# Performance work log

Hardware: AMD Instinct MI355X
Metric: run time of the kernel (lower is better)

Reference implementation:

```python
import jax, jax.numpy as jnp
import numpy as np

B, L, D, H = 2, 2048, 1024, 16
DK = D // H


def setup_inputs() -> dict:
    key = jax.random.key(0)
    ks = jax.random.split(key, 11)
    s = 1.0 / np.sqrt(D)
    inp = {
        "context_sequence": jax.random.normal(ks[0], (B, L, D), jnp.float32),
        "value_sequence": jax.random.normal(ks[1], (B, L, D), jnp.float32),
        "mask": jnp.tril(jnp.ones((L, L), jnp.int32)),  # causal mask [L, L]
        "Wq": jax.random.normal(ks[2], (D, D), jnp.float32) * s,
        "bq": jax.random.normal(ks[3], (D,), jnp.float32) * s,
        "Wk": jax.random.normal(ks[4], (D, D), jnp.float32) * s,
        "bk": jax.random.normal(ks[5], (D,), jnp.float32) * s,
        "Wv": jax.random.normal(ks[6], (D, D), jnp.float32) * s,
        "bv": jax.random.normal(ks[7], (D,), jnp.float32) * s,
        "Wo": jax.random.normal(ks[8], (D, D), jnp.float32) * s,
        "bo": jax.random.normal(ks[9], (D,), jnp.float32) * s,
    }
    return inp


def reference(context_sequence, value_sequence, mask, Wq, bq, Wk, bk, Wv, bv, Wo, bo):
    orig_dtype = context_sequence.dtype
    # QKV projections; Q,K from context, V from value stream
    Q = (context_sequence @ Wq + bq).reshape(B, L, H, DK)
    K = (context_sequence @ Wk + bk).reshape(B, L, H, DK)
    V = (value_sequence @ Wv + bv).reshape(B, L, H, DK)
    # fp32 QK^T with 1/sqrt(d_k) scaling -> [B, H, L, L]
    scores = jnp.einsum("bqhd,bkhd->bhqk", Q.astype(jnp.float32), K.astype(jnp.float32)) / jnp.sqrt(
        jnp.asarray(DK, jnp.float32)
    )
    # dtype-dependent neg fill (fp32 -> -inf); causal rows always have >=1 valid entry
    neg_fill = jnp.asarray(-jnp.inf, jnp.float32)
    scores = jnp.where(mask[None, None, :, :] == 0, neg_fill, scores)
    scores = scores.astype(orig_dtype)
    attn = jax.nn.softmax(scores, axis=-1)
    # dropout is identity in eval mode
    out = jnp.einsum("bhqk,bkhd->bqhd", attn, V).reshape(B, L, D)
    return out @ Wo + bo
```

## Files before the change

### kernel.cpp

```cpp
#include <hip/hip_runtime.h>
#include <hip/hip_bf16.h>
#include <stdint.h>

#define B_   2
#define L_   2048
#define D_   1024
#define H_   16
#define DK_  64

typedef __attribute__((ext_vector_type(4))) float f32x4;
typedef __attribute__((ext_vector_type(8))) short short8;
typedef unsigned short ushort_t;

__device__ __forceinline__ ushort_t f2bf(float f) {
    union { float f; uint32_t u; } v; v.f = f;
    uint32_t r = v.u + 0x7FFFu + ((v.u >> 16) & 1u);
    return (ushort_t)(r >> 16);
}
__device__ __forceinline__ float bf2f(ushort_t u) {
    union { uint32_t u; float f; } v; v.u = (uint32_t)u << 16; return v.f;
}
__device__ __forceinline__ uint32_t pack_bf16_rne(float a, float b) {
    return (uint32_t)f2bf(a) | ((uint32_t)f2bf(b) << 16);
}

__device__ __forceinline__ void async_copy16(void* lds, const void* g) {
    __builtin_amdgcn_global_load_lds(
        (const __attribute__((address_space(1))) uint32_t*)g,
        (__attribute__((address_space(3))) uint32_t*)lds, 16, 0, 0);
}

__global__ void prep_kernel(const float* __restrict__ ctx, const float* __restrict__ val,
                            const float* __restrict__ w0, const float* __restrict__ w1,
                            const float* __restrict__ w2, const float* __restrict__ w3,
                            ushort_t* __restrict__ xc, ushort_t* __restrict__ xv,
                            ushort_t* __restrict__ wt) {
    __shared__ float tile[32][33];
    const int bid = blockIdx.x;
    if (bid < 8192) {
        const float* s = (bid >= 4096) ? val : ctx;
        ushort_t*    d = (bid >= 4096) ? xv : xc;
        int i = ((bid & 4095) * 256 + threadIdx.x) * 4;
        float4 v = *(const float4*)(s + i);
        ushort4 o;
        o.x = f2bf(v.x); o.y = f2bf(v.y); o.z = f2bf(v.z); o.w = f2bf(v.w);
        *(ushort4*)(d + i) = o;
    } else {
        const int t = bid - 8192;
        const int z = t >> 10;
        const int rem = t & 1023;
        const int by = rem >> 5, bx = rem & 31;
        const float* w = (z == 0) ? w0 : (z == 1) ? w1 : (z == 2) ? w2 : w3;
        ushort_t* o = wt + (size_t)z * D_ * D_;
        const int tx = threadIdx.x & 31, ty = threadIdx.x >> 5;
        const int k0 = by * 32, d0 = bx * 32;
#pragma unroll
        for (int i = 0; i < 4; i++)
            tile[ty + i * 8][tx] = w[(size_t)(k0 + ty + i * 8) * D_ + d0 + tx];
        __syncthreads();
#pragma unroll
        for (int i = 0; i < 4; i++)
            o[(size_t)(d0 + ty + i * 8) * D_ + k0 + tx] = f2bf(tile[tx][ty + i * 8]);
    }
}

template <bool SWAP>
__device__ __forceinline__ void gemm_main(const ushort_t* __restrict__ A,
                                          const ushort_t* __restrict__ WT,
                                          char* smem, int m0, int n0, int tid,
                                          f32x4 (&acc)[4][4]) {
    const int wid = tid >> 6, lane = tid & 63;
    const int wm = (wid >> 1) * 64, wn = (wid & 1) * 64;
#pragma unroll
    for (int i = 0; i < 4; i++)
#pragma unroll
        for (int j = 0; j < 4; j++) { f32x4 z = {0.f, 0.f, 0.f, 0.f}; acc[i][j] = z; }

    auto stage = [&](int buf, int k0) {
        char* bA = smem + buf * 32768;
        char* bB = bA + 16384;
#pragma unroll
        for (int i = 0; i < 4; i++) {
            int flat = i * 256 + tid; int row = flat >> 3; int win = (flat & 7) * 16;
            const char* srcA = (const char*)A + ((size_t)(m0 + row) * D_ + k0) * 2 + (win ^ ((row & 7) << 4));
            async_copy16(bA + (i * 256 + wid * 64) * 16, srcA);
            const char* srcB = (const char*)WT + ((size_t)(n0 + row) * D_ + k0) * 2 + (win ^ ((row & 7) << 4));
            async_copy16(bB + (i * 256 + wid * 64) * 16, srcB);
        }
    };

    stage(0, 0);
    int cur = 0;
    for (int k0 = 0; k0 < D_; k0 += 64) {
        __syncthreads();
        if (k0 + 64 < D_) stage(cur ^ 1, k0 + 64);
        const char* bA = smem + cur * 32768;
        const char* bB = bA + 16384;
#pragma unroll
        for (int ks = 0; ks < 2; ks++) {
            short8 af[4], bf[4];
            int kb = ks * 64 + ((lane >> 4) << 4);
#pragma unroll
            for (int t = 0; t < 4; t++) {
                int ml = wm + t * 16 + (lane & 15);
                af[t] = *(const short8*)(bA + ml * 128 + (kb ^ ((ml & 7) << 4)));
                int nl = wn + t * 16 + (lane & 15);
                bf[t] = *(const short8*)(bB + nl * 128 + (kb ^ ((nl & 7) << 4)));
            }
#pragma unroll
            for (int mt = 0; mt < 4; mt++)
#pragma unroll
                for (int nt = 0; nt < 4; nt++)
                    acc[mt][nt] = SWAP
                        ? __builtin_amdgcn_mfma_f32_16x16x32_bf16(bf[nt], af[mt], acc[mt][nt], 0, 0, 0)
                        : __builtin_amdgcn_mfma_f32_16x16x32_bf16(af[mt], bf[nt], acc[mt][nt], 0, 0, 0);
        }
        cur ^= 1;
    }
}

__device__ __forceinline__ void gemm_main8(const ushort_t* __restrict__ A,
                                           const ushort_t* __restrict__ WT,
                                           char* smem, int m0, int n0, int tid,
                                           f32x4 (&acc)[4][2]) {
    const int wid = tid >> 6, lane = tid & 63;
    const int wm = (wid >> 2) * 64, wn = (wid & 3) * 32;
#pragma unroll
    for (int i = 0; i < 4; i++)
#pragma unroll
        for (int j = 0; j < 2; j++) { f32x4 z = {0.f, 0.f, 0.f, 0.f}; acc[i][j] = z; }

    auto stage = [&](int buf, int k0) {
        char* bA = smem + buf * 32768;
        char* bB = bA + 16384;
#pragma unroll
        for (int i = 0; i < 2; i++) {
            int flat = i * 512 + tid; int row = flat >> 3; int win = (flat & 7) * 16;
            const char* srcA = (const char*)A + ((size_t)(m0 + row) * D_ + k0) * 2 + (win ^ ((row & 7) << 4));
            async_copy16(bA + (i * 512 + wid * 64) * 16, srcA);
            const char* srcB = (const char*)WT + ((size_t)(n0 + row) * D_ + k0) * 2 + (win ^ ((row & 7) << 4));
            async_copy16(bB + (i * 512 + wid * 64) * 16, srcB);
        }
    };

    stage(0, 0);
    int cur = 0;
    for (int k0 = 0; k0 < D_; k0 += 64) {
        __syncthreads();
        if (k0 + 64 < D_) stage(cur ^ 1, k0 + 64);
        const char* bA = smem + cur * 32768;
        const char* bB = bA + 16384;
#pragma unroll
        for (int ks = 0; ks < 2; ks++) {
            short8 af[4], bf[2];
            int kb = ks * 64 + ((lane >> 4) << 4);
#pragma unroll
            for (int t = 0; t < 4; t++) {
                int ml = wm + t * 16 + (lane & 15);
                af[t] = *(const short8*)(bA + ml * 128 + (kb ^ ((ml & 7) << 4)));
            }
#pragma unroll
            for (int t = 0; t < 2; t++) {
                int nl = wn + t * 16 + (lane & 15);
                bf[t] = *(const short8*)(bB + nl * 128 + (kb ^ ((nl & 7) << 4)));
            }
#pragma unroll
            for (int mt = 0; mt < 4; mt++)
#pragma unroll
                for (int nt = 0; nt < 2; nt++)
                    acc[mt][nt] = __builtin_amdgcn_mfma_f32_16x16x32_bf16(bf[nt], af[mt], acc[mt][nt], 0, 0, 0);
        }
        cur ^= 1;
    }
}

#define QSCALE 0.18033688f

__global__ __launch_bounds__(256, 2) void gemm_qkv(
    const ushort_t* __restrict__ Xc, const ushort_t* __restrict__ Xv,
    const ushort_t* __restrict__ WT0,
    const float* __restrict__ bq, const float* __restrict__ bk, const float* __restrict__ bv,
    ushort_t* __restrict__ qw, ushort_t* __restrict__ kw, ushort_t* __restrict__ vtw) {
    __shared__ __align__(16) char smem[65536];
    const int z = blockIdx.z;
    const ushort_t* A  = (z == 2) ? Xv : Xc;
    const ushort_t* WT = WT0 + (size_t)z * D_ * D_;
    const float* bias  = (z == 0) ? bq : (z == 1) ? bk : bv;
    const int tid = threadIdx.x, wid = tid >> 6, lane = tid & 63;
    const int lo = lane & 15, hi = lane >> 4;
    const int m0 = blockIdx.y * 128, n0 = blockIdx.x * 128;
    const int wm = (wid >> 1) * 64, wn = (wid & 1) * 64;
    f32x4 acc[4][4];
    if (z != 2) {
        gemm_main<true>(A, WT, smem, m0, n0, tid, acc);
#pragma unroll
        for (int mt = 0; mt < 4; mt++)
#pragma unroll
            for (int nt = 0; nt < 4; nt++) {
                int m  = m0 + wm + mt * 16 + lo;
                int nb = n0 + wn + nt * 16 + 4 * hi;
                float4 b4 = *(const float4*)(bias + nb);
                float v0 = acc[mt][nt][0] + b4.x;
                float v1 = acc[mt][nt][1] + b4.y;
                float v2 = acc[mt][nt][2] + b4.z;
                float v3 = acc[mt][nt][3] + b4.w;
                if (z == 0) { v0 *= QSCALE; v1 *= QSCALE; v2 *= QSCALE; v3 *= QSCALE; }
                int b = m >> 11, tok = m & 2047, h = nb >> 6, dk = nb & 63;
                uint2 w;
                w.x = pack_bf16_rne(v0, v1);
                w.y = pack_bf16_rne(v2, v3);
                ushort_t* outp = (z == 0) ? qw : kw;
                *(uint2*)(outp + ((size_t)(b * H_ + h) * L_ + tok) * DK_ + dk) = w;
            }
    } else {
        gemm_main<false>(A, WT, smem, m0, n0, tid, acc);
#pragma unroll
        for (int mt = 0; mt < 4; mt++)
#pragma unroll
            for (int nt = 0; nt < 4; nt++) {
                int n  = n0 + wn + nt * 16 + lo;
                int mb = m0 + wm + mt * 16 + 4 * hi;
                float bv_ = bias[n];
                int b = mb >> 11, tok = mb & 2047, h = n >> 6, dk = n & 63;
                uint2 w;
                w.x = pack_bf16_rne(acc[mt][nt][0] + bv_, acc[mt][nt][1] + bv_);
                w.y = pack_bf16_rne(acc[mt][nt][2] + bv_, acc[mt][nt][3] + bv_);
                *(uint2*)(vtw + ((size_t)(b * H_ + h) * DK_ + dk) * L_ + tok) = w;
            }
    }
}

__global__ __launch_bounds__(512, 2) void gemm_out(
    const ushort_t* __restrict__ O, const ushort_t* __restrict__ WT,
    const float* __restrict__ bo, float* __restrict__ out) {
    __shared__ __align__(16) char smem[65536];
    const int tid = threadIdx.x, wid = tid >> 6, lane = tid & 63;
    const int lo = lane & 15, hi = lane >> 4;
    const int m0 = blockIdx.y * 128, n0 = blockIdx.x * 128;
    const int wm = (wid >> 2) * 64, wn = (wid & 3) * 32;
    f32x4 acc[4][2];
    gemm_main8(O, WT, smem, m0, n0, tid, acc);
#pragma unroll
    for (int mt = 0; mt < 4; mt++)
#pragma unroll
        for (int nt = 0; nt < 2; nt++) {
            int m  = m0 + wm + mt * 16 + lo;
            int nb = n0 + wn + nt * 16 + 4 * hi;
            float4 b4 = *(const float4*)(bo + nb);
            float4 o;
            o.x = acc[mt][nt][0] + b4.x;
            o.y = acc[mt][nt][1] + b4.y;
            o.z = acc[mt][nt][2] + b4.z;
            o.w = acc[mt][nt][3] + b4.w;
            *(float4*)(out + (size_t)m * D_ + nb) = o;
        }
}

__global__ __launch_bounds__(512, 2) void attn_kernel(
    const ushort_t* __restrict__ qws, const ushort_t* __restrict__ kws,
    const ushort_t* __restrict__ vtws, ushort_t* __restrict__ ows) {
    __shared__ __align__(16) char smem[67584];
    const int tid = threadIdx.x, wid = tid >> 6, lane = tid & 63;
    const int lo = lane & 15, hi = lane >> 4;
    const int bid = blockIdx.x;
    const int xcd = bid & 7, slot = bid >> 3;
    const int bh = xcd * 4 + (slot >> 4);
    const int pi = slot & 15;
    char* P0 = smem + wid * 8192;
    float* lall = (float*)(smem + 65536);
    float* lw = lall + wid * 64;
    const int swz = (lo & 7) << 4;

    short8 ones;
#pragma unroll
    for (int i = 0; i < 8; i++) ones[i] = (short)0x3F80;
    const f32x4 minit = {-32.f, -32.f, -32.f, -32.f};

#pragma unroll 1
    for (int half = 0; half < 2; half++) {
        const int qtb = half ? (31 - pi) : pi;
        const int Q0 = qtb * 64;
        const int ntiles = qtb + 1;

        short8 qf[4][2];
#pragma unroll
        for (int qt = 0; qt < 4; qt++)
#pragma unroll
            for (int ks = 0; ks < 2; ks++)
                qf[qt][ks] = *(const short8*)(qws + (size_t)(bh * L_ + Q0 + qt * 16 + lo) * DK_ + ks * 32 + hi * 8);

        f32x4 oa[4][4];
        f32x4 lf4[4];
#pragma unroll
        for (int qt = 0; qt < 4; qt++) {
            f32x4 z = {0.f, 0.f, 0.f, 0.f};
            lf4[qt] = z;
#pragma unroll
            for (int ot = 0; ot < 4; ot++) oa[qt][ot] = z;
        }

#pragma unroll 1
        for (int t = wid; t < ntiles; t += 8) {
            const int k0 = t * 64;
            const bool diag = (t == qtb);
            short8 vf[4][2];
#pragma unroll
            for (int ot = 0; ot < 4; ot++)
#pragma unroll
                for (int ks = 0; ks < 2; ks++)
                    vf[ot][ks] = *(const short8*)(vtws + (size_t)(bh * DK_ + ot * 16 + lo) * L_ + k0 + ks * 32 + hi * 8);
#pragma unroll
            for (int kt = 0; kt < 4; kt++) {
                const ushort_t* krow = kws + (size_t)(bh * L_ + k0 + kt * 16 + lo) * DK_ + hi * 8;
                short8 kf0 = *(const short8*)(krow);
                short8 kf1 = *(const short8*)(krow + 32);
                const int kb = kt * 16 + 4 * hi;
#pragma unroll
                for (int qt = 0; qt < 4; qt++) {
                    f32x4 s = __builtin_amdgcn_mfma_f32_16x16x32_bf16(kf0, qf[qt][0], minit, 0, 0, 0);
                    s = __builtin_amdgcn_mfma_f32_16x16x32_bf16(kf1, qf[qt][1], s, 0, 0, 0);
                    float p0 = __builtin_amdgcn_exp2f(s[0]);
                    float p1 = __builtin_amdgcn_exp2f(s[1]);
                    float p2 = __builtin_amdgcn_exp2f(s[2]);
                    float p3 = __builtin_amdgcn_exp2f(s[3]);
                    if (diag) {
                        const int qg = qt * 16 + lo;
                        p0 = (kb > qg)     ? 0.f : p0;
                        p1 = (kb + 1 > qg) ? 0.f : p1;
                        p2 = (kb + 2 > qg) ? 0.f : p2;
                        p3 = (kb + 3 > qg) ? 0.f : p3;
                    }
                    uint2 w;
                    w.x = __builtin_amdgcn_perm(__float_as_uint(p1), __float_as_uint(p0), 0x07060302u);
                    w.y = __builtin_amdgcn_perm(__float_as_uint(p3), __float_as_uint(p2), 0x07060302u);
                    *(uint2*)(P0 + qt * 2048 + lo * 128 + ((kt * 32 + hi * 8) ^ swz)) = w;
                }
            }
            __builtin_amdgcn_s_setprio(1);
#pragma unroll
            for (int qt = 0; qt < 4; qt++)
#pragma unroll
                for (int ks = 0; ks < 2; ks++) {
                    short8 pf = *(const short8*)(P0 + qt * 2048 + lo * 128 + ((ks * 64 + hi * 16) ^ swz));
                    lf4[qt] = __builtin_amdgcn_mfma_f32_16x16x32_bf16(pf, ones, lf4[qt], 0, 0, 0);
#pragma unroll
                    for (int ot = 0; ot < 4; ot++)
                        oa[qt][ot] = __builtin_amdgcn_mfma_f32_16x16x32_bf16(pf, vf[ot][ks], oa[qt][ot], 0, 0, 0);
                }
            __builtin_amdgcn_s_setprio(0);
        }

#pragma unroll
        for (int qt = 0; qt < 4; qt++)
#pragma unroll
            for (int ot = 0; ot < 4; ot++)
#pragma unroll
                for (int r = 0; r < 4; r++) {
                    int row = qt * 16 + 4 * hi + r;
                    *(ushort_t*)(P0 + row * 128 + (((ot * 16 + lo) * 2) ^ ((row & 7) << 4))) = f2bf(oa[qt][ot][r]);
                }
        if (lo == 0) {
#pragma unroll
            for (int qt = 0; qt < 4; qt++)
                *(f32x4*)(lw + qt * 16 + 4 * hi) = lf4[qt];
        }
        __syncthreads();

        {
            const int q = tid >> 3, c = tid & 7;
            float acc[8];
#pragma unroll
            for (int e = 0; e < 8; e++) acc[e] = 0.f;
#pragma unroll
            for (int w = 0; w < 8; w++) {
                short8 a = *(const short8*)(smem + w * 8192 + q * 128 + ((c * 16) ^ ((q & 7) << 4)));
#pragma unroll
                for (int e = 0; e < 8; e++) acc[e] += bf2f((ushort_t)a[e]);
            }
            float ls = 0.f;
#pragma unroll
            for (int w = 0; w < 8; w++) ls += lall[w * 64 + q];
            float ri = 1.0f / ls;
            short8 o;
#pragma unroll
            for (int e = 0; e < 8; e++) o[e] = (short)f2bf(acc[e] * ri);
            size_t ob = (size_t)((bh >> 4) * L_ + Q0 + q) * D_ + (bh & 15) * DK_ + c * 8;
            *(short8*)(ows + ob) = o;
        }
        __syncthreads();
    }
}

extern "C" void kernel_launch(void* const* d_in, const int* in_sizes, int n_in,
                              void* d_out, int out_size, void* d_ws, size_t ws_size,
                              hipStream_t stream) {
    (void)in_sizes; (void)n_in; (void)out_size; (void)ws_size;
    const float* ctx = (const float*)d_in[0];
    const float* val = (const float*)d_in[1];
    const float* Wq = (const float*)d_in[3];
    const float* bq = (const float*)d_in[4];
    const float* Wk = (const float*)d_in[5];
    const float* bk = (const float*)d_in[6];
    const float* Wv = (const float*)d_in[7];
    const float* bv = (const float*)d_in[8];
    const float* Wo = (const float*)d_in[9];
    const float* bo = (const float*)d_in[10];
    float* out = (float*)d_out;

    char* ws = (char*)d_ws;
    ushort_t* xc  = (ushort_t*)(ws);
    ushort_t* xv  = (ushort_t*)(ws + 8388608);
    ushort_t* wt  = (ushort_t*)(ws + 16777216);
    ushort_t* qws = (ushort_t*)(ws + 25165824);
    ushort_t* kws = (ushort_t*)(ws + 33554432);
    ushort_t* vtw = (ushort_t*)(ws + 41943040);

    prep_kernel<<<dim3(12288), 256, 0, stream>>>(ctx, val, Wq, Wk, Wv, Wo, xc, xv, wt);
    gemm_qkv<<<dim3(8, 32, 3), 256, 0, stream>>>(xc, xv, wt, bq, bk, bv, qws, kws, vtw);
    attn_kernel<<<dim3(512), 512, 0, stream>>>(qws, kws, vtw, xc );
    gemm_out<<<dim3(8, 32), 512, 0, stream>>>(xc, wt + (size_t)3 * D_ * D_, bo, out);
}
```

Measured before the change: 125.5 us.

## Split attention KV tiles across two blocks and combine partials in new kernel

The attention kernel now launches twice as many blocks of 256 threads. Each block covers every other KV tile for its query tile and writes unnormalized bf16 partial outputs plus per-row softmax denominators to workspace. A new combine_o kernel sums the two partials, normalizes them and writes the head-interleaved O that the output GEMM reads. The aim is smaller blocks with cheaper block-wide syncs and LDS reductions, paid for by an extra launch, extra global partial traffic and an extra bf16 rounding of the partial sums.

```diff
diff --git a/kernel.cpp b/kernel.cpp
--- a/kernel.cpp
+++ b/kernel.cpp
@@ -256,18 +256,20 @@
         }
 }
 
-__global__ __launch_bounds__(512, 2) void attn_kernel(
+__global__ __launch_bounds__(256, 2) void attn_kernel(
     const ushort_t* __restrict__ qws, const ushort_t* __restrict__ kws,
-    const ushort_t* __restrict__ vtws, ushort_t* __restrict__ ows) {
-    __shared__ __align__(16) char smem[67584];
+    const ushort_t* __restrict__ vtws,
+    ushort_t* __restrict__ pO0, ushort_t* __restrict__ pO1, float* __restrict__ lp) {
+    __shared__ __align__(16) char smem[33792];
     const int tid = threadIdx.x, wid = tid >> 6, lane = tid & 63;
     const int lo = lane & 15, hi = lane >> 4;
     const int bid = blockIdx.x;
-    const int xcd = bid & 7, slot = bid >> 3;
-    const int bh = xcd * 4 + (slot >> 4);
-    const int pi = slot & 15;
+    const int xcd = bid & 7;
+    const int sk  = (bid >> 3) & 1;
+    const int pi  = (bid >> 4) & 15;
+    const int bh  = xcd * 4 + (bid >> 8);
     char* P0 = smem + wid * 8192;
-    float* lall = (float*)(smem + 65536);
+    float* lall = (float*)(smem + 32768);
     float* lw = lall + wid * 64;
     const int swz = (lo & 7) << 4;
 
@@ -300,7 +302,7 @@
         }
 
 #pragma unroll 1
-        for (int t = wid; t < ntiles; t += 8) {
+        for (int t = (wid << 1) | sk; t < ntiles; t += 8) {
             const int k0 = t * 64;
             const bool diag = (t == qtb);
             short8 vf[4][2];
@@ -367,28 +369,55 @@
         __syncthreads();
 
         {
-            const int q = tid >> 3, c = tid & 7;
-            float acc[8];
-#pragma unroll
-            for (int e = 0; e < 8; e++) acc[e] = 0.f;
-#pragma unroll
-            for (int w = 0; w < 8; w++) {
-                short8 a = *(const short8*)(smem + w * 8192 + q * 128 + ((c * 16) ^ ((q & 7) << 4)));
-#pragma unroll
-                for (int e = 0; e < 8; e++) acc[e] += bf2f((ushort_t)a[e]);
+            const int q = tid >> 2, c = tid & 3;
+            float acc[16];
+#pragma unroll
+            for (int j = 0; j < 16; j++) acc[j] = 0.f;
+#pragma unroll
+            for (int w = 0; w < 4; w++) {
+                const char* base = smem + w * 8192 + q * 128;
+                short8 a = *(const short8*)(base + ((c * 32)      ^ ((q & 7) << 4)));
+                short8 b = *(const short8*)(base + ((c * 32 + 16) ^ ((q & 7) << 4)));
+#pragma unroll
+                for (int j = 0; j < 8; j++) acc[j]     += bf2f((ushort_t)a[j]);
+#pragma unroll
+                for (int j = 0; j < 8; j++) acc[8 + j] += bf2f((ushort_t)b[j]);
             }
             float ls = 0.f;
 #pragma unroll
-            for (int w = 0; w < 8; w++) ls += lall[w * 64 + q];
-            float ri = 1.0f / ls;
-            short8 o;
-#pragma unroll
-            for (int e = 0; e < 8; e++) o[e] = (short)f2bf(acc[e] * ri);
-            size_t ob = (size_t)((bh >> 4) * L_ + Q0 + q) * D_ + (bh & 15) * DK_ + c * 8;
-            *(short8*)(ows + ob) = o;
+            for (int w = 0; w < 4; w++) ls += lall[w * 64 + q];
+            short8 o0, o1;
+#pragma unroll
+            for (int j = 0; j < 8; j++) o0[j] = (short)f2bf(acc[j]);
+#pragma unroll
+            for (int j = 0; j < 8; j++) o1[j] = (short)f2bf(acc[8 + j]);
+            ushort_t* part = sk ? pO1 : pO0;
+            size_t pb = (((size_t)(bh * 32 + qtb) * 64) + q) * 64 + c * 16;
+            *(short8*)(part + pb)     = o0;
+            *(short8*)(part + pb + 8) = o1;
+            if (c == 0) lp[((size_t)(bh * 32 + qtb) * 2 + sk) * 64 + q] = ls;
         }
         __syncthreads();
     }
+}
+
+__global__ void combine_o(const ushort_t* __restrict__ O0, const ushort_t* __restrict__ O1,
+                          const float* __restrict__ lp, ushort_t* __restrict__ outO) {
+    const int bid = blockIdx.x;
+    const int xcd = bid & 7, rest = bid >> 3;
+    const int bh = xcd * 4 + (rest >> 6);
+    const int f  = (rest & 63) * 256 + threadIdx.x;
+    const int qtb = f >> 9, q = (f >> 3) & 63, dk8 = f & 7;
+    size_t pb = (((size_t)(bh * 32 + qtb) * 64) + q) * 64 + dk8 * 8;
+    short8 a = *(const short8*)(O0 + pb);
+    short8 b = *(const short8*)(O1 + pb);
+    size_t lb = ((size_t)(bh * 32 + qtb) * 2) * 64 + q;
+    float ri = 1.0f / (lp[lb] + lp[lb + 64]);
+    short8 o;
+#pragma unroll
+    for (int e = 0; e < 8; e++) o[e] = (short)f2bf((bf2f((ushort_t)a[e]) + bf2f((ushort_t)b[e])) * ri);
+    size_t ob = ((size_t)(bh >> 4) * L_ + qtb * 64 + q) * D_ + (bh & 15) * DK_ + dk8 * 8;
+    *(short8*)(outO + ob) = o;
 }
 
 extern "C" void kernel_launch(void* const* d_in, const int* in_sizes, int n_in,
@@ -414,9 +443,11 @@
     ushort_t* qws = (ushort_t*)(ws + 25165824);
     ushort_t* kws = (ushort_t*)(ws + 33554432);
     ushort_t* vtw = (ushort_t*)(ws + 41943040);
+    float*    lpt = (float*)(ws + 16777216);
 
     prep_kernel<<<dim3(12288), 256, 0, stream>>>(ctx, val, Wq, Wk, Wv, Wo, xc, xv, wt);
     gemm_qkv<<<dim3(8, 32, 3), 256, 0, stream>>>(xc, xv, wt, bq, bk, bv, qws, kws, vtw);
-    attn_kernel<<<dim3(512), 512, 0, stream>>>(qws, kws, vtw, xc );
-    gemm_out<<<dim3(8, 32), 512, 0, stream>>>(xc, wt + (size_t)3 * D_ * D_, bo, out);
-}
+    attn_kernel<<<dim3(1024), 256, 0, stream>>>(qws, kws, vtw, xv , xc , lpt);
+    combine_o<<<dim3(2048), 256, 0, stream>>>(xv, xc, lpt, qws );
+    gemm_out<<<dim3(8, 32), 512, 0, stream>>>(qws, wt + (size_t)3 * D_ * D_, bo, out);
+}
```

Result: slower. 131.7 us (+4.9%).
